# Kernel optimization log

Measured on AMD Instinct MI355X. Metric: run time of the kernel, lower is better.

The kernel has to match this reference:

```python
import math
import jax, jax.numpy as jnp
import numpy as np


def get_alibi_slopes(n_heads: int) -> jnp.ndarray:
    def _pow2_slopes(n):
        i = jnp.arange(1, n + 1, dtype=jnp.float32)
        return jnp.power(2.0, -8.0 * i / n)
    if n_heads & (n_heads - 1) == 0:
        return _pow2_slopes(n_heads)
    nearest = 2 ** math.ceil(math.log2(n_heads))
    full = _pow2_slopes(nearest)
    half = nearest // 2
    half_slopes = _pow2_slopes(half)
    extra = full[jnp.arange(half) * 2 + 1]
    return jnp.concatenate([half_slopes, extra])[:n_heads]


def build_alibi_bias(n_heads: int, T: int, causal: bool = True) -> jnp.ndarray:
    slopes = get_alibi_slopes(n_heads)  # (H,)
    idx = jnp.arange(T)
    rel = jnp.abs(idx[:, None] - idx[None, :]).astype(jnp.float32)  # (T,T)
    bias = -slopes[:, None, None] * rel[None]  # (H,T,T)
    if causal:
        future = idx[None, :] > idx[:, None]
        bias = jnp.where(future[None], -jnp.inf, bias)
    return bias


def setup_inputs() -> dict:
    key = jax.random.key(0)
    ks = jax.random.split(key, 5)
    B, T, C = 2, 2048, 1024
    s = 0.02
    return {
        "x": jax.random.normal(ks[0], (B, T, C), dtype=jnp.float32),
        "Wq": jax.random.normal(ks[1], (C, C), dtype=jnp.float32) * s,
        "Wk": jax.random.normal(ks[2], (C, C), dtype=jnp.float32) * s,
        "Wv": jax.random.normal(ks[3], (C, C), dtype=jnp.float32) * s,
        "Wo": jax.random.normal(ks[4], (C, C), dtype=jnp.float32) * s,
    }


def reference(x, Wq, Wk, Wv, Wo):
    B, T, C = x.shape
    H = 16
    D = C // H
    scale = D ** -0.5
    # torch nn.Linear(bias=False): y = x @ W.T
    def proj_split(W):
        t = jnp.einsum('btc,dc->btd', x, W)
        return t.reshape(B, T, H, D).transpose(0, 2, 1, 3)  # (B,H,T,D)
    q, k, v = proj_split(Wq), proj_split(Wk), proj_split(Wv)
    scores = jnp.einsum('bhtd,bhsd->bhts', q, k) * scale  # (B,H,T,T)
    bias = build_alibi_bias(H, T, causal=True)  # (H,T,T)
    scores = scores + bias[None]
    attn = jax.nn.softmax(scores, axis=-1)
    out = jnp.einsum('bhts,bhsd->bhtd', attn, v)
    out = out.transpose(0, 2, 1, 3).reshape(B, T, C)
    return jnp.einsum('btc,dc->btd', out, Wo)
```

## Files before the change

kernel.cpp:

```cpp
#include <hip/hip_runtime.h>
#include <hip/hip_bf16.h>


typedef _Float16 f16;
typedef f16 f16x2 __attribute__((ext_vector_type(2)));
typedef f16 f16x4 __attribute__((ext_vector_type(4)));
typedef f16 f16x8 __attribute__((ext_vector_type(8)));
typedef float f32x4 __attribute__((ext_vector_type(4)));

#define LOG2E 1.4426950408889634f
#define LDA 72
#define LDV 132

typedef const __attribute__((address_space(1))) unsigned int* gas1;
typedef __attribute__((address_space(3))) unsigned int* las3;
__device__ __forceinline__ void gload16(const f16* g, f16* l) {
  __builtin_amdgcn_global_load_lds((gas1)g, (las3)l, 16, 0, 0);
}

__device__ __forceinline__ f16x4 pk4(f32x4 v) {
  f16x2 a = __builtin_bit_cast(f16x2, __builtin_amdgcn_cvt_pkrtz(v[0], v[1]));
  f16x2 b = __builtin_bit_cast(f16x2, __builtin_amdgcn_cvt_pkrtz(v[2], v[3]));
  f16x4 r; r[0] = a[0]; r[1] = a[1]; r[2] = b[0]; r[3] = b[1];
  return r;
}

__global__ __launch_bounds__(256) void cvt_f32_f16(
    const float* __restrict__ x, const float* __restrict__ wq,
    const float* __restrict__ wk, const float* __restrict__ wv,
    const float* __restrict__ wo,
    f16* __restrict__ dx, f16* __restrict__ dwq, f16* __restrict__ dwk,
    f16* __restrict__ dwv, f16* __restrict__ dwo) {
  const float* src; f16* dst; int n;
  switch (blockIdx.y) {
    case 0:  src = x;  dst = dx;  n = 4194304; break;
    case 1:  src = wq; dst = dwq; n = 1048576; break;
    case 2:  src = wk; dst = dwk; n = 1048576; break;
    case 3:  src = wv; dst = dwv; n = 1048576; break;
    default: src = wo; dst = dwo; n = 1048576; break;
  }
  int i = (blockIdx.x * 256 + (int)threadIdx.x) * 8;
  if (i >= n) return;
  f32x4 a = *(const f32x4*)(src + i);
  f32x4 b = *(const f32x4*)(src + i + 4);
  f16x8 o;
  f16x4 lo4 = pk4(a), hi4 = pk4(b);
#pragma unroll
  for (int j = 0; j < 4; j++) { o[j] = lo4[j]; o[j + 4] = hi4[j]; }
  *(f16x8*)(dst + i) = o;
}

__device__ __forceinline__ void gemm_core(const f16* __restrict__ A,
                                          const f16* __restrict__ W,
                                          int m0, int n0,
                                          f16* lA, f16* lW,
                                          f32x4 acc[4][4]) {
  const int tid = threadIdx.x;
  const int lane = tid & 63, w = tid >> 6;
  const int wm = w & 1, wn = w >> 1;
  const int q = lane & 15, quad = lane >> 4;
  const int lrow = lane >> 2, lcol = (lane & 3) * 8;

  for (int kt = 0; kt < 1024; kt += 32) {
    __syncthreads();
#pragma unroll
    for (int t = 0; t < 2; t++) {
      const int slot = t * 4 + w;
      const int row = slot * 16 + lrow;
      gload16(A + (m0 + row) * 1024 + kt + lcol, lA + slot * 512);
      gload16(W + (n0 + row) * 1024 + kt + lcol, lW + slot * 512);
    }
    __syncthreads();
    f16x8 aF[4], bF[4];
#pragma unroll
    for (int mt = 0; mt < 4; mt++)
      aF[mt] = *(const f16x8*)(lA + (wm * 64 + mt * 16 + q) * 32 + quad * 8);
#pragma unroll
    for (int nt = 0; nt < 4; nt++)
      bF[nt] = *(const f16x8*)(lW + (wn * 64 + nt * 16 + q) * 32 + quad * 8);
#pragma unroll
    for (int mt = 0; mt < 4; mt++)
#pragma unroll
      for (int nt = 0; nt < 4; nt++)
        acc[mt][nt] = __builtin_amdgcn_mfma_f32_16x16x32_f16(aF[mt], bF[nt], acc[mt][nt], 0, 0, 0);
  }
}

__global__ __launch_bounds__(256) void qkv_proj(
    const f16* __restrict__ x16, const f16* __restrict__ wq16,
    const f16* __restrict__ wk16, const f16* __restrict__ wv16,
    f16* __restrict__ qb, f16* __restrict__ kb, f16* __restrict__ vb,
    float qscale) {
  __shared__ __align__(16) f16 lA[128 * 32];
  __shared__ __align__(16) f16 lW[128 * 32];
  const int m0 = blockIdx.x * 128, n0 = blockIdx.y * 128;
  const int z = blockIdx.z;
  const f16* W = (z == 0) ? wq16 : (z == 1) ? wk16 : wv16;
  f16* out = (z == 0) ? qb : (z == 1) ? kb : vb;
  const float scale = (z == 0) ? qscale : 1.0f;

  f32x4 acc[4][4];
  const f32x4 zero = {0.f, 0.f, 0.f, 0.f};
#pragma unroll
  for (int i = 0; i < 4; i++)
#pragma unroll
    for (int j = 0; j < 4; j++) acc[i][j] = zero;
  gemm_core(x16, W, m0, n0, lA, lW, acc);

  const int tid = threadIdx.x, lane = tid & 63, w = tid >> 6;
  const int wm = w & 1, wn = w >> 1, q = lane & 15, quad = lane >> 4;
#pragma unroll
  for (int mt = 0; mt < 4; mt++)
#pragma unroll
    for (int nt = 0; nt < 4; nt++) {
      int n = n0 + wn * 64 + nt * 16 + q;
      int h = n >> 6, d = n & 63;
#pragma unroll
      for (int r = 0; r < 4; r++) {
        int mm = m0 + wm * 64 + mt * 16 + quad * 4 + r;
        int bb = mm >> 11, tl = mm & 2047;
        out[((bb * 16 + h) * 2048 + tl) * 64 + d] = (f16)(acc[mt][nt][r] * scale);
      }
    }
}

__global__ __launch_bounds__(512) void attn(
    const f16* __restrict__ qB, const f16* __restrict__ kB,
    const f16* __restrict__ vB, f16* __restrict__ att) {
  __shared__ __align__(16) f16 lK[128 * LDA];
  __shared__ __align__(16) f16 lV[64 * LDV];
  const int tid = threadIdx.x, lane = tid & 63, w = tid >> 6;
  const int q = lane & 15, quad = lane >> 4;
  const int qb_ = 15 - (int)blockIdx.x, bh = blockIdx.y;
  const int b = bh >> 4, h = bh & 15;
  const int q0 = qb_ * 128;
  const f16* qP = qB + (bh * 2048) * 64;
  const f16* kP = kB + (bh * 2048) * 64;
  const f16* vP = vB + (bh * 2048) * 64;

  const float slope2 = __builtin_amdgcn_exp2f(-0.5f * (float)(h + 1)) * LOG2E;
  const int qg = q0 + w * 16 + q;
  const int diag_kvh = q0 + (w >> 2) * 64;

  f16x8 qF[2];
#pragma unroll
  for (int ks = 0; ks < 2; ks++)
    qF[ks] = *(const f16x8*)(qP + qg * 64 + ks * 32 + quad * 8);

  const f32x4 cinit = {-8.f, -8.f, -8.f, -8.f};
  f32x4 ot[4];
#pragma unroll
  for (int i = 0; i < 4; i++) ot[i] = {0.f, 0.f, 0.f, 0.f};
  float lsum = 0.0f;

  const int kr = tid >> 3, ks8 = (tid & 7) * 8;
  const int vp = (tid & 63) * 2, vd = (tid >> 6) * 8;

  f16x8 kreg[2], vreg[2];
#pragma unroll
  for (int it = 0; it < 2; it++)
    kreg[it] = *(const f16x8*)(kP + (it * 64 + kr) * 64 + ks8);
#pragma unroll
  for (int r2 = 0; r2 < 2; r2++)
    vreg[r2] = *(const f16x8*)(vP + (vp + r2) * 64 + vd);

  const int nstage = qb_ + 1;
  for (int st = 0; st < nstage; st++) {
    const int kv0 = st << 7;
    __syncthreads();
#pragma unroll
    for (int it = 0; it < 2; it++)
      *(f16x8*)(lK + (it * 64 + kr) * LDA + ks8) = kreg[it];
#pragma unroll
    for (int j = 0; j < 8; j++) {
      f16x2 t; t[0] = vreg[0][j]; t[1] = vreg[1][j];
      *(f16x2*)(lV + (vd + j) * LDV + vp) = t;
    }
    __syncthreads();
    if (st + 1 < nstage) {
      const int kn = kv0 + 128;
#pragma unroll
      for (int it = 0; it < 2; it++)
        kreg[it] = *(const f16x8*)(kP + (kn + it * 64 + kr) * 64 + ks8);
#pragma unroll
      for (int r2 = 0; r2 < 2; r2++)
        vreg[r2] = *(const f16x8*)(vP + (kn + vp + r2) * 64 + vd);
    }
#pragma unroll
    for (int half = 0; half < 2; half++) {
      const int kvh = kv0 + half * 64;
      if (kvh > diag_kvh) break;
      f32x4 stv[4];
#pragma unroll
      for (int sub = 0; sub < 4; sub++) {
        const f16* kb_ = lK + (half * 64 + sub * 16 + q) * LDA + quad * 8;
        f16x8 k0 = *(const f16x8*)(kb_);
        f16x8 k1 = *(const f16x8*)(kb_ + 32);
        f32x4 a = __builtin_amdgcn_mfma_f32_16x16x32_f16(k0, qF[0], cinit, 0, 0, 0);
        a = __builtin_amdgcn_mfma_f32_16x16x32_f16(k1, qF[1], a, 0, 0, 0);
        stv[sub] = a;
      }
      const int dQ = qg - kvh;
      const bool needmask = (kvh == diag_kvh);
      f16x4 pF[4];
#pragma unroll
      for (int sub = 0; sub < 4; sub++) {
        f32x4 ev;
#pragma unroll
        for (int r = 0; r < 4; r++) {
          float dd = (float)(dQ - (sub * 16 + quad * 4 + r));
          float val = fmaf(-slope2, dd, stv[sub][r]);
          if (needmask) val = (dd >= 0.0f) ? val : -3e38f;
          ev[r] = __builtin_amdgcn_exp2f(val);
        }
        lsum += (ev[0] + ev[1]) + (ev[2] + ev[3]);
        pF[sub] = pk4(ev);
      }
#pragma unroll
      for (int sub = 0; sub < 4; sub++)
#pragma unroll
        for (int dt = 0; dt < 4; dt++) {
          f16x4 vF = *(const f16x4*)(lV + (dt * 16 + q) * LDV + half * 64 + sub * 16 + quad * 4);
          ot[dt] = __builtin_amdgcn_mfma_f32_16x16x16f16(vF, pF[sub], ot[dt], 0, 0, 0);
        }
    }
  }

  lsum += __shfl_xor(lsum, 16);
  lsum += __shfl_xor(lsum, 32);
  const float inv = 1.0f / lsum;

  __syncthreads();
  f16* OT = lK + w * (16 * LDA);
#pragma unroll
  for (int dt = 0; dt < 4; dt++) {
    f16x4 o4;
#pragma unroll
    for (int r = 0; r < 4; r++) o4[r] = (f16)(ot[dt][r] * inv);
    *(f16x4*)(OT + q * LDA + dt * 16 + quad * 4) = o4;
  }
  __syncthreads();
  const int row = lane >> 2, cs = lane & 3;
  f16x8 o8a = *(const f16x8*)(OT + row * LDA + cs * 16);
  f16x8 o8b = *(const f16x8*)(OT + row * LDA + cs * 16 + 8);
  f16* dst = att + (b * 2048 + q0 + w * 16 + row) * 1024 + h * 64 + cs * 16;
  *(f16x8*)dst = o8a;
  *(f16x8*)(dst + 8) = o8b;
}

__global__ __launch_bounds__(256) void out_proj(
    const f16* __restrict__ att, const f16* __restrict__ wo16,
    float* __restrict__ out) {
  __shared__ __align__(16) f16 lA[128 * 32];
  __shared__ __align__(16) f16 lW[128 * 32];
  const int m0 = blockIdx.x * 128, n0 = blockIdx.y * 128;
  f32x4 acc[4][4];
  const f32x4 zero = {0.f, 0.f, 0.f, 0.f};
#pragma unroll
  for (int i = 0; i < 4; i++)
#pragma unroll
    for (int j = 0; j < 4; j++) acc[i][j] = zero;
  gemm_core(att, wo16, m0, n0, lA, lW, acc);

  const int tid = threadIdx.x, lane = tid & 63, w = tid >> 6;
  const int wm = w & 1, wn = w >> 1, q = lane & 15, quad = lane >> 4;
#pragma unroll
  for (int mt = 0; mt < 4; mt++)
#pragma unroll
    for (int nt = 0; nt < 4; nt++) {
      int n = n0 + wn * 64 + nt * 16 + q;
#pragma unroll
      for (int r = 0; r < 4; r++) {
        int mm = m0 + wm * 64 + mt * 16 + quad * 4 + r;
        out[mm * 1024 + n] = acc[mt][nt][r];
      }
    }
}

extern "C" void kernel_launch(void* const* d_in, const int* in_sizes, int n_in,
                              void* d_out, int out_size, void* d_ws, size_t ws_size,
                              hipStream_t stream) {
  const float* x  = (const float*)d_in[0];
  const float* Wq = (const float*)d_in[1];
  const float* Wk = (const float*)d_in[2];
  const float* Wv = (const float*)d_in[3];
  const float* Wo = (const float*)d_in[4];
  char* ws = (char*)d_ws;
  const size_t MB = 1024 * 1024;
  f16* x16  = (f16*)(ws);
  f16* qb   = (f16*)(ws + 8 * MB);
  f16* kb   = (f16*)(ws + 16 * MB);
  f16* vb   = (f16*)(ws + 24 * MB);
  f16* wq16 = (f16*)(ws + 32 * MB);
  f16* wk16 = (f16*)(ws + 34 * MB);
  f16* wv16 = (f16*)(ws + 36 * MB);
  f16* wo16 = (f16*)(ws + 38 * MB);
  f16* att  = x16;

  cvt_f32_f16<<<dim3(2048, 5), 256, 0, stream>>>(x, Wq, Wk, Wv, Wo,
                                                 x16, wq16, wk16, wv16, wo16);
  qkv_proj<<<dim3(32, 8, 3), 256, 0, stream>>>(x16, wq16, wk16, wv16,
                                               qb, kb, vb, 0.125f * LOG2E);
  attn<<<dim3(16, 32), 512, 0, stream>>>(qb, kb, vb, att);
  out_proj<<<dim3(32, 8), 256, 0, stream>>>(att, wo16, (float*)d_out);
}
```

Before: 202.6 us.

## Rewrite attention kernel with 32x32x16 MFMA tiles and 4-wave blocks

The attention kernel moves from 16x16 MFMA tiles with 8 waves per block (16 query rows each) to 32x32x16 MFMA with 4 waves per block (32 query rows each). K rows are permuted in LDS so the score accumulator layout feeds straight into the PV MFMA operand, and the second 32-key sub-tile is skipped when it lies entirely above the causal diagonal. The grid is reordered so heads vary fastest, and the V LDS stride changes. Larger MFMA tiles should cut instruction count and LDS traffic per FLOP, at the cost of more registers per wave and fewer waves per block.

```diff
diff --git a/kernel.cpp b/kernel.cpp
--- a/kernel.cpp
+++ b/kernel.cpp
@@ -7,10 +7,11 @@
 typedef f16 f16x4 __attribute__((ext_vector_type(4)));
 typedef f16 f16x8 __attribute__((ext_vector_type(8)));
 typedef float f32x4 __attribute__((ext_vector_type(4)));
+typedef float f32x16 __attribute__((ext_vector_type(16)));
 
 #define LOG2E 1.4426950408889634f
 #define LDA 72
-#define LDV 132
+#define LDV 136
 
 typedef const __attribute__((address_space(1))) unsigned int* gas1;
 typedef __attribute__((address_space(3))) unsigned int* las3;
@@ -22,6 +23,16 @@
   f16x2 a = __builtin_bit_cast(f16x2, __builtin_amdgcn_cvt_pkrtz(v[0], v[1]));
   f16x2 b = __builtin_bit_cast(f16x2, __builtin_amdgcn_cvt_pkrtz(v[2], v[3]));
   f16x4 r; r[0] = a[0]; r[1] = a[1]; r[2] = b[0]; r[3] = b[1];
+  return r;
+}
+__device__ __forceinline__ f16x8 mkp(const float* e, int p) {
+  f16x2 a = __builtin_bit_cast(f16x2, __builtin_amdgcn_cvt_pkrtz(e[4*p+0], e[4*p+1]));
+  f16x2 b = __builtin_bit_cast(f16x2, __builtin_amdgcn_cvt_pkrtz(e[4*p+2], e[4*p+3]));
+  f16x2 c = __builtin_bit_cast(f16x2, __builtin_amdgcn_cvt_pkrtz(e[8+4*p+0], e[8+4*p+1]));
+  f16x2 d = __builtin_bit_cast(f16x2, __builtin_amdgcn_cvt_pkrtz(e[8+4*p+2], e[8+4*p+3]));
+  f16x8 r;
+  r[0]=a[0]; r[1]=a[1]; r[2]=b[0]; r[3]=b[1];
+  r[4]=c[0]; r[5]=c[1]; r[6]=d[0]; r[7]=d[1];
   return r;
 }
 
@@ -124,14 +135,14 @@
     }
 }
 
-__global__ __launch_bounds__(512) void attn(
+__global__ __launch_bounds__(256) void attn(
     const f16* __restrict__ qB, const f16* __restrict__ kB,
     const f16* __restrict__ vB, f16* __restrict__ att) {
   __shared__ __align__(16) f16 lK[128 * LDA];
   __shared__ __align__(16) f16 lV[64 * LDV];
   const int tid = threadIdx.x, lane = tid & 63, w = tid >> 6;
-  const int q = lane & 15, quad = lane >> 4;
-  const int qb_ = 15 - (int)blockIdx.x, bh = blockIdx.y;
+  const int n5 = lane & 31, hh = lane >> 5;
+  const int bh = blockIdx.x, qb_ = 15 - (int)blockIdx.y;
   const int b = bh >> 4, h = bh & 15;
   const int q0 = qb_ * 128;
   const f16* qP = qB + (bh * 2048) * 64;
@@ -139,113 +150,164 @@
   const f16* vP = vB + (bh * 2048) * 64;
 
   const float slope2 = __builtin_amdgcn_exp2f(-0.5f * (float)(h + 1)) * LOG2E;
-  const int qg = q0 + w * 16 + q;
-  const int diag_kvh = q0 + (w >> 2) * 64;
-
-  f16x8 qF[2];
-#pragma unroll
-  for (int ks = 0; ks < 2; ks++)
-    qF[ks] = *(const f16x8*)(qP + qg * 64 + ks * 32 + quad * 8);
-
-  const f32x4 cinit = {-8.f, -8.f, -8.f, -8.f};
-  f32x4 ot[4];
-#pragma unroll
-  for (int i = 0; i < 4; i++) ot[i] = {0.f, 0.f, 0.f, 0.f};
+  const int qg = q0 + w * 32 + n5;
+  const int qlast = q0 + w * 32 + 31;
+  const int wdiag = ((q0 + w * 32) >> 6) << 6;
+
+  f16x8 qF[4];
+#pragma unroll
+  for (int ks = 0; ks < 4; ks++)
+    qF[ks] = *(const f16x8*)(qP + qg * 64 + ks * 16 + hh * 8);
+
+  f32x16 cinit, ot0, ot1;
+#pragma unroll
+  for (int i = 0; i < 16; i++) { cinit[i] = -8.0f; ot0[i] = 0.f; ot1[i] = 0.f; }
   float lsum = 0.0f;
 
-  const int kr = tid >> 3, ks8 = (tid & 7) * 8;
-  const int vp = (tid & 63) * 2, vd = (tid >> 6) * 8;
-
-  f16x8 kreg[2], vreg[2];
-#pragma unroll
-  for (int it = 0; it < 2; it++)
-    kreg[it] = *(const f16x8*)(kP + (it * 64 + kr) * 64 + ks8);
-#pragma unroll
-  for (int r2 = 0; r2 < 2; r2++)
-    vreg[r2] = *(const f16x8*)(vP + (vp + r2) * 64 + vd);
+  const int kr = tid >> 2, kc = (tid & 3) * 8;
+  const int pp = kr & 31;
+  const int mperm = (pp & 3) + 16 * ((pp >> 2) & 1) + 4 * ((pp >> 3) & 1) + 8 * ((pp >> 4) & 1);
+  const int lkr = (kr & 32) + mperm;
+  const int vp = (tid & 63) * 2, vd0 = (tid >> 6) * 8;
+
+  f16x8 kA0, kA1, kB0, kB1, vA0, vA1, vB0, vB1;
+  kA0 = *(const f16x8*)(kP + kr * 64 + kc);
+  kA1 = *(const f16x8*)(kP + kr * 64 + kc + 32);
+  kB0 = *(const f16x8*)(kP + (64 + kr) * 64 + kc);
+  kB1 = *(const f16x8*)(kP + (64 + kr) * 64 + kc + 32);
+  vA0 = *(const f16x8*)(vP + vp * 64 + vd0);
+  vA1 = *(const f16x8*)(vP + (vp + 1) * 64 + vd0);
+  vB0 = *(const f16x8*)(vP + vp * 64 + vd0 + 32);
+  vB1 = *(const f16x8*)(vP + (vp + 1) * 64 + vd0 + 32);
 
   const int nstage = qb_ + 1;
-  for (int st = 0; st < nstage; st++) {
-    const int kv0 = st << 7;
+  for (int stg = 0; stg < nstage; stg++) {
+    const int kv0 = stg << 7;
     __syncthreads();
-#pragma unroll
-    for (int it = 0; it < 2; it++)
-      *(f16x8*)(lK + (it * 64 + kr) * LDA + ks8) = kreg[it];
+    *(f16x8*)(lK + lkr * LDA + kc) = kA0;
+    *(f16x8*)(lK + lkr * LDA + kc + 32) = kA1;
+    *(f16x8*)(lK + (64 + lkr) * LDA + kc) = kB0;
+    *(f16x8*)(lK + (64 + lkr) * LDA + kc + 32) = kB1;
 #pragma unroll
     for (int j = 0; j < 8; j++) {
-      f16x2 t; t[0] = vreg[0][j]; t[1] = vreg[1][j];
-      *(f16x2*)(lV + (vd + j) * LDV + vp) = t;
+      f16x2 t0; t0[0] = vA0[j]; t0[1] = vA1[j];
+      *(f16x2*)(lV + (vd0 + j) * LDV + vp) = t0;
+      f16x2 t1; t1[0] = vB0[j]; t1[1] = vB1[j];
+      *(f16x2*)(lV + (vd0 + 32 + j) * LDV + vp) = t1;
     }
     __syncthreads();
-    if (st + 1 < nstage) {
+    if (stg + 1 < nstage) {
       const int kn = kv0 + 128;
-#pragma unroll
-      for (int it = 0; it < 2; it++)
-        kreg[it] = *(const f16x8*)(kP + (kn + it * 64 + kr) * 64 + ks8);
-#pragma unroll
-      for (int r2 = 0; r2 < 2; r2++)
-        vreg[r2] = *(const f16x8*)(vP + (kn + vp + r2) * 64 + vd);
+      kA0 = *(const f16x8*)(kP + (kn + kr) * 64 + kc);
+      kA1 = *(const f16x8*)(kP + (kn + kr) * 64 + kc + 32);
+      kB0 = *(const f16x8*)(kP + (kn + 64 + kr) * 64 + kc);
+      kB1 = *(const f16x8*)(kP + (kn + 64 + kr) * 64 + kc + 32);
+      vA0 = *(const f16x8*)(vP + (kn + vp) * 64 + vd0);
+      vA1 = *(const f16x8*)(vP + (kn + vp + 1) * 64 + vd0);
+      vB0 = *(const f16x8*)(vP + (kn + vp) * 64 + vd0 + 32);
+      vB1 = *(const f16x8*)(vP + (kn + vp + 1) * 64 + vd0 + 32);
     }
 #pragma unroll
     for (int half = 0; half < 2; half++) {
       const int kvh = kv0 + half * 64;
-      if (kvh > diag_kvh) break;
-      f32x4 stv[4];
-#pragma unroll
-      for (int sub = 0; sub < 4; sub++) {
-        const f16* kb_ = lK + (half * 64 + sub * 16 + q) * LDA + quad * 8;
-        f16x8 k0 = *(const f16x8*)(kb_);
-        f16x8 k1 = *(const f16x8*)(kb_ + 32);
-        f32x4 a = __builtin_amdgcn_mfma_f32_16x16x32_f16(k0, qF[0], cinit, 0, 0, 0);
-        a = __builtin_amdgcn_mfma_f32_16x16x32_f16(k1, qF[1], a, 0, 0, 0);
-        stv[sub] = a;
-      }
-      const int dQ = qg - kvh;
-      const bool needmask = (kvh == diag_kvh);
-      f16x4 pF[4];
-#pragma unroll
-      for (int sub = 0; sub < 4; sub++) {
-        f32x4 ev;
-#pragma unroll
-        for (int r = 0; r < 4; r++) {
-          float dd = (float)(dQ - (sub * 16 + quad * 4 + r));
-          float val = fmaf(-slope2, dd, stv[sub][r]);
-          if (needmask) val = (dd >= 0.0f) ? val : -3e38f;
-          ev[r] = __builtin_amdgcn_exp2f(val);
+      if (kvh > wdiag) break;
+      const bool act1 = (kvh + 32 <= qlast);
+      const bool needmask = (kvh == wdiag);
+      f32x16 s0 = cinit, s1 = cinit;
+#pragma unroll
+      for (int ks = 0; ks < 4; ks++) {
+        f16x8 kf = *(const f16x8*)(lK + (half * 64 + n5) * LDA + ks * 16 + hh * 8);
+        s0 = __builtin_amdgcn_mfma_f32_32x32x16_f16(kf, qF[ks], s0, 0, 0, 0);
+      }
+      if (act1) {
+#pragma unroll
+        for (int ks = 0; ks < 4; ks++) {
+          f16x8 kf = *(const f16x8*)(lK + (half * 64 + 32 + n5) * LDA + ks * 16 + hh * 8);
+          s1 = __builtin_amdgcn_mfma_f32_32x32x16_f16(kf, qF[ks], s1, 0, 0, 0);
         }
-        lsum += (ev[0] + ev[1]) + (ev[2] + ev[3]);
-        pF[sub] = pk4(ev);
-      }
-#pragma unroll
-      for (int sub = 0; sub < 4; sub++)
-#pragma unroll
-        for (int dt = 0; dt < 4; dt++) {
-          f16x4 vF = *(const f16x4*)(lV + (dt * 16 + q) * LDV + half * 64 + sub * 16 + quad * 4);
-          ot[dt] = __builtin_amdgcn_mfma_f32_16x16x16f16(vF, pF[sub], ot[dt], 0, 0, 0);
+      }
+      f16x8 pf00, pf01, pf10, pf11;
+      {
+        const int dQ = qg - kvh - 8 * hh;
+        const float base0 = -slope2 * (float)dQ;
+        float ev[16];
+#pragma unroll
+        for (int u = 0; u < 4; u++)
+#pragma unroll
+          for (int t = 0; t < 4; t++) {
+            const int reg = t + 4 * u;
+            const int CR = 16 * (u & 1) + 4 * (u >> 1) + t;
+            float val = s0[reg] + fmaf(slope2, (float)CR, base0);
+            if (needmask) val = (dQ >= CR) ? val : -1e30f;
+            float e = __builtin_amdgcn_exp2f(val);
+            lsum += e;
+            ev[reg] = e;
+          }
+        pf00 = mkp(ev, 0); pf01 = mkp(ev, 1);
+        if (act1) {
+          const int dQ1 = dQ - 32;
+          const float base1 = -slope2 * (float)dQ1;
+          float ev1[16];
+#pragma unroll
+          for (int u = 0; u < 4; u++)
+#pragma unroll
+            for (int t = 0; t < 4; t++) {
+              const int reg = t + 4 * u;
+              const int CR = 16 * (u & 1) + 4 * (u >> 1) + t;
+              float val = s1[reg] + fmaf(slope2, (float)CR, base1);
+              if (needmask) val = (dQ1 >= CR) ? val : -1e30f;
+              float e = __builtin_amdgcn_exp2f(val);
+              lsum += e;
+              ev1[reg] = e;
+            }
+          pf10 = mkp(ev1, 0); pf11 = mkp(ev1, 1);
         }
+      }
+#pragma unroll
+      for (int p = 0; p < 2; p++) {
+        f16x8 vf0 = *(const f16x8*)(lV + n5 * LDV + half * 64 + p * 16 + hh * 8);
+        f16x8 vf1 = *(const f16x8*)(lV + (32 + n5) * LDV + half * 64 + p * 16 + hh * 8);
+        f16x8 pf = p ? pf01 : pf00;
+        ot0 = __builtin_amdgcn_mfma_f32_32x32x16_f16(vf0, pf, ot0, 0, 0, 0);
+        ot1 = __builtin_amdgcn_mfma_f32_32x32x16_f16(vf1, pf, ot1, 0, 0, 0);
+      }
+      if (act1) {
+#pragma unroll
+        for (int p = 0; p < 2; p++) {
+          f16x8 vf0 = *(const f16x8*)(lV + n5 * LDV + half * 64 + 32 + p * 16 + hh * 8);
+          f16x8 vf1 = *(const f16x8*)(lV + (32 + n5) * LDV + half * 64 + 32 + p * 16 + hh * 8);
+          f16x8 pf = p ? pf11 : pf10;
+          ot0 = __builtin_amdgcn_mfma_f32_32x32x16_f16(vf0, pf, ot0, 0, 0, 0);
+          ot1 = __builtin_amdgcn_mfma_f32_32x32x16_f16(vf1, pf, ot1, 0, 0, 0);
+        }
+      }
     }
   }
 
-  lsum += __shfl_xor(lsum, 16);
   lsum += __shfl_xor(lsum, 32);
   const float inv = 1.0f / lsum;
 
   __syncthreads();
-  f16* OT = lK + w * (16 * LDA);
-#pragma unroll
-  for (int dt = 0; dt < 4; dt++) {
-    f16x4 o4;
-#pragma unroll
-    for (int r = 0; r < 4; r++) o4[r] = (f16)(ot[dt][r] * inv);
-    *(f16x4*)(OT + q * LDA + dt * 16 + quad * 4) = o4;
-  }
+  f16* OT = lK + w * (32 * LDA);
+#pragma unroll
+  for (int dt = 0; dt < 2; dt++)
+#pragma unroll
+    for (int u = 0; u < 4; u++) {
+      f16x4 o4;
+#pragma unroll
+      for (int t = 0; t < 4; t++) {
+        float v = (dt ? ot1[t + 4 * u] : ot0[t + 4 * u]) * inv;
+        o4[t] = (f16)v;
+      }
+      *(f16x4*)(OT + n5 * LDA + dt * 32 + 8 * u + 4 * hh) = o4;
+    }
   __syncthreads();
-  const int row = lane >> 2, cs = lane & 3;
-  f16x8 o8a = *(const f16x8*)(OT + row * LDA + cs * 16);
-  f16x8 o8b = *(const f16x8*)(OT + row * LDA + cs * 16 + 8);
-  f16* dst = att + (b * 2048 + q0 + w * 16 + row) * 1024 + h * 64 + cs * 16;
-  *(f16x8*)dst = o8a;
-  *(f16x8*)(dst + 8) = o8b;
+  const int row = lane >> 1, hr = lane & 1;
+  const f16* OR = lK + w * (32 * LDA) + row * LDA + hr * 32;
+  f16* dst = att + (b * 2048 + q0 + w * 32 + row) * 1024 + h * 64 + hr * 32;
+#pragma unroll
+  for (int j = 0; j < 4; j++)
+    *(f16x8*)(dst + j * 8) = *(const f16x8*)(OR + j * 8);
 }
 
 __global__ __launch_bounds__(256) void out_proj(
@@ -301,6 +363,6 @@
                                                  x16, wq16, wk16, wv16, wo16);
   qkv_proj<<<dim3(32, 8, 3), 256, 0, stream>>>(x16, wq16, wk16, wv16,
                                                qb, kb, vb, 0.125f * LOG2E);
-  attn<<<dim3(16, 32), 512, 0, stream>>>(qb, kb, vb, att);
+  attn<<<dim3(32, 16), 256, 0, stream>>>(qb, kb, vb, att);
   out_proj<<<dim3(32, 8), 256, 0, stream>>>(att, wo16, (float*)d_out);
 }
```

Result: faster. 186.6 us (-7.9%).
